# Kernel tuning notes

Hardware: AMD Instinct MI355X
Metric: run time of the kernel (lower is better)

Reference implementation:

```python
import jax, jax.numpy as jnp
import numpy as np

HEAD_DIM = 128
N_HEADS = 16
N_KV_HEADS = 4
ROPE_BASE = 10000.0
TRAIN_SEQ_LEN = 1024


def _rotary_cos_sin(seq_len, rd, base=ROPE_BASE, train_len=TRAIN_SEQ_LEN):
    # NTK-style base scaling when seq_len exceeds training length (matches Rotary.forward)
    if seq_len > train_len:
        scale = seq_len / train_len
        base = base * scale ** (rd / (rd - 2))
    inv_freq = 1.0 / base ** (np.arange(0, rd, 2, dtype=np.float32) / rd)
    freqs = np.outer(np.arange(seq_len, dtype=np.float32), inv_freq)  # [T, rd/2]
    cos = jnp.asarray(np.cos(freqs))[None, :, None, :]  # [1,T,1,rd/2]
    sin = jnp.asarray(np.sin(freqs))[None, :, None, :]
    return cos, sin


def _apply_rotary(x, cos, sin):
    h = x.shape[-1] // 2
    x1, x2 = x[..., :h], x[..., h:]
    return jnp.concatenate((x1 * cos + x2 * sin, -x1 * sin + x2 * cos), axis=-1)


def _rms_norm(x):
    eps = jnp.finfo(x.dtype).eps
    return x * jax.lax.rsqrt(jnp.mean(x * x, axis=-1, keepdims=True) + eps)


def setup_inputs() -> dict:
    key = jax.random.key(0)
    ks = jax.random.split(key, 6)
    B, T, D = 4, 2048, 2048
    x = jax.random.normal(ks[0], (B, T, D), dtype=jnp.float32)
    q_w = jax.random.normal(ks[1], (D, D), dtype=jnp.float32) * 0.02
    k_w = jax.random.normal(ks[2], (N_KV_HEADS * HEAD_DIM, D), dtype=jnp.float32) * 0.02
    v_w = jax.random.normal(ks[3], (N_KV_HEADS * HEAD_DIM, D), dtype=jnp.float32) * 0.02
    out_w = jax.random.normal(ks[4], (D, D), dtype=jnp.float32) * 0.02
    q_gain = jnp.ones((N_HEADS,), dtype=jnp.float32)
    return {"x": x, "q_w": q_w, "k_w": k_w, "v_w": v_w, "out_w": out_w, "q_gain": q_gain}


def reference(x, q_w, k_w, v_w, out_w, q_gain):
    B, T, D = x.shape
    q = (x @ q_w.T).reshape(B, T, N_HEADS, HEAD_DIM)
    k = (x @ k_w.T).reshape(B, T, N_KV_HEADS, HEAD_DIM)
    v = (x @ v_w.T).reshape(B, T, N_KV_HEADS, HEAD_DIM)
    q = _rms_norm(q)
    k = _rms_norm(k)
    cos, sin = _rotary_cos_sin(T, HEAD_DIM)
    q = _apply_rotary(q, cos, sin)
    k = _apply_rotary(k, cos, sin)
    q = q * q_gain[None, None, :, None]
    # GQA: expand kv heads (repeat_interleave semantics)
    rep = N_HEADS // N_KV_HEADS
    k = jnp.repeat(k, rep, axis=2)  # [B,T,H,D]
    v = jnp.repeat(v, rep, axis=2)
    scale = 1.0 / jnp.sqrt(jnp.asarray(HEAD_DIM, dtype=x.dtype))
    scores = jnp.einsum("bthd,bshd->bhts", q, k) * scale  # [B,H,T,T]
    causal = jnp.tril(jnp.ones((T, T), dtype=bool))
    scores = jnp.where(causal[None, None], scores, jnp.asarray(-jnp.inf, dtype=scores.dtype))
    w = jax.nn.softmax(scores, axis=-1)
    y = jnp.einsum("bhts,bshd->bthd", w, v).reshape(B, T, D)
    return y @ out_w.T
```

## Files before the change

### kernel.cpp

```cpp
#include <hip/hip_runtime.h>
#include <hip/hip_bf16.h>
#include <math.h>

#define HEAD_DIM 128
#define NH 16
#define NKV 4
#define BB 4
#define TT 2048
#define DD 2048
#define ROWS (BB*TT)

typedef unsigned short u16;
typedef unsigned int u32;
typedef __attribute__((ext_vector_type(8))) short short8;
typedef __attribute__((ext_vector_type(4))) float f32x4;
typedef __attribute__((ext_vector_type(16))) float f32x16;
typedef __attribute__((ext_vector_type(4))) unsigned short u16x4;

__device__ __forceinline__ float bf2f(u16 u) {
    union { unsigned int i; float f; } v; v.i = ((unsigned int)u) << 16; return v.f;
}
__device__ __forceinline__ u16 f2bf(float f) {
    union { float f; unsigned int i; } v; v.f = f;
    unsigned int r = v.i + 0x7FFFu + ((v.i >> 16) & 1u);
    return (u16)(r >> 16);
}
__device__ __forceinline__ f32x4 mfma16(short8 a, short8 b, f32x4 c) {
    return __builtin_amdgcn_mfma_f32_16x16x32_bf16(a, b, c, 0, 0, 0);
}
__device__ __forceinline__ f32x16 mfma32(short8 a, short8 b, f32x16 c) {
    return __builtin_amdgcn_mfma_f32_32x32x16_bf16(a, b, c, 0, 0, 0);
}
__device__ __forceinline__ f32x16 zero16() {
    f32x16 z;
    #pragma unroll
    for (int i = 0; i < 16; ++i) z[i] = 0.f;
    return z;
}
__device__ __forceinline__ void gload_lds16(const u16* g, u16* l) {
    __builtin_amdgcn_global_load_lds(
        (const __attribute__((address_space(1))) unsigned int*)(const void*)g,
        (__attribute__((address_space(3))) unsigned int*)(void*)l, 16, 0, 0);
}

__global__ __launch_bounds__(256)
void cast_f2b(const float* __restrict__ in, u16* __restrict__ out, int n)
{
    int i = (blockIdx.x * 256 + threadIdx.x) * 4;
    if (i >= n) return;
    float4 v = *(const float4*)(in + i);
    u16x4 o;
    o.x = f2bf(v.x); o.y = f2bf(v.y); o.z = f2bf(v.z); o.w = f2bf(v.w);
    *(u16x4*)(out + i) = o;
}

__global__ __launch_bounds__(256)
void prep_all(const float* __restrict__ x,  const float* __restrict__ qw,
              const float* __restrict__ kw, const float* __restrict__ vw,
              u16* __restrict__ xh, u16* __restrict__ wq, u16* __restrict__ wkv,
              float* __restrict__ cs, float* __restrict__ sn, float base)
{
    const int bid = blockIdx.x, tid = threadIdx.x;
    if (bid < 22528) {
        const float* src; u16* dst; int i4;
        if (bid < 16384)      { src = x;  dst = xh;            i4 = bid; }
        else if (bid < 20480) { src = qw; dst = wq;            i4 = bid - 16384; }
        else if (bid < 21504) { src = kw; dst = wkv;           i4 = bid - 20480; }
        else                  { src = vw; dst = wkv + 1048576; i4 = bid - 21504; }
        int i = (i4 * 256 + tid) * 4;
        float4 v = *(const float4*)(src + i);
        u16x4 o;
        o.x = f2bf(v.x); o.y = f2bf(v.y); o.z = f2bf(v.z); o.w = f2bf(v.w);
        *(u16x4*)(dst + i) = o;
    } else {
        int idx = (bid - 22528) * 256 + tid;
        int t = idx >> 6;
        int d = idx & 63;
        float inv = powf(base, -(float)(2 * d) / 128.0f);
        float f = (float)t * inv;
        cs[idx] = cosf(f);
        sn[idx] = sinf(f);
    }
}

__global__ __launch_bounds__(256)
void transpose_v(const u16* __restrict__ vbh, u16* __restrict__ vtb)
{
    __shared__ u16 tile[64][72];
    const int tb = blockIdx.x;
    const int db = blockIdx.y;
    const int z  = blockIdx.z;
    const int tid = threadIdx.x;

    {
        const int r = tid >> 2, cq = tid & 3;
        const u16* src = vbh + ((size_t)(((z >> 2) * TT + tb * 64 + r) * NKV + (z & 3))) * 128
                             + db * 64 + cq * 16;
        short8 s0 = *(const short8*)(src);
        short8 s1 = *(const short8*)(src + 8);
        #pragma unroll
        for (int e = 0; e < 8; ++e) tile[r][cq * 16 + e]     = (u16)s0[e];
        #pragma unroll
        for (int e = 0; e < 8; ++e) tile[r][cq * 16 + 8 + e] = (u16)s1[e];
    }
    __syncthreads();
    {
        const int d = tid >> 2, tq = tid & 3;
        __attribute__((aligned(16))) u16 tmp[16];
        #pragma unroll
        for (int e = 0; e < 16; ++e) {
            int esw = (e & 3) | ((e & 4) << 1) | ((e & 8) >> 1);
            tmp[e] = tile[tq * 16 + esw][d];
        }
        u16* dst = vtb + (((size_t)(z * (TT / 64) + tb) * 128 + (db * 64 + d)) << 6) + tq * 16;
        *(short8*)(dst)     = ((short8*)tmp)[0];
        *(short8*)(dst + 8) = ((short8*)tmp)[1];
    }
}

template<int BN, int OUTMODE>
__global__ __launch_bounds__(512, 2)
void gemm256(const u16* __restrict__ A, const u16* __restrict__ W,
             void* __restrict__ C0, void* __restrict__ C1,
             const float* __restrict__ CS, const float* __restrict__ SN,
             const float* __restrict__ GAIN, float PRE)
{
    constexpr int WN    = (BN == 256) ? 4 : 2;
    constexpr int MR    = (BN == 256) ? 8 : 4;
    constexpr int WROW  = (BN == 256) ? 128 : 64;
    constexpr int NT    = DD / 64;
    constexpr int NBI   = (BN == 256) ? 4 : 2;
    constexpr int BPR   = BN / 16;

    __shared__ u16 LDSall[2 * 128 * 128 + 2 * (BN / 2) * 128];
    __shared__ float Sred[1024];
    u16* AsL = LDSall;
    u16* BsL = LDSall + 2 * 128 * 128;

    const int tid = threadIdx.x;
    const int w = tid >> 6, l = tid & 63;
    const int lq = l & 15, lg = l >> 4;
    const int wmi = (WN == 4) ? (w >> 2) : (w >> 1);
    const int wni = w & (WN - 1);

    int bmi, bni;
    {
        const int bid = blockIdx.x;
        const int wg = (bid & 7) * 32 + (bid >> 3);
        const int st = wg >> 2, wi = wg & 3;
        const int sty = st >> 2, stx = st & 3;
        bmi = sty * 2 + (wi >> 1);
        bni = stx * 2 + (wi & 1);
    }
    const int bm = bmi * 256, bn = bni * BN;

    const int sro = l >> 4;
    const int sch = l & 15;

    f32x4 acc[MR][4];
    #pragma unroll
    for (int m = 0; m < MR; ++m)
        #pragma unroll
        for (int n = 0; n < 4; ++n) acc[m][n] = (f32x4){0.f, 0.f, 0.f, 0.f};

    auto stage = [&](int buf, int t) {
        const size_t ko = (size_t)t * 64;
        u16* Ad = AsL + buf * (128 * 128);
        u16* Bd = BsL + buf * ((BN / 2) * 128);
        #pragma unroll
        for (int j = 0; j < 4; ++j) {
            int rp = w * 16 + j * 4 + sro;
            int cg = sch ^ (rp & 15);
            gload_lds16(A + (size_t)(bm + 2 * rp + (cg >> 3)) * DD + ko + (cg & 7) * 8,
                        Ad + (w * 16 + j * 4) * 128);
        }
        #pragma unroll
        for (int j = 0; j < NBI; ++j) {
            int rp = w * BPR + j * 4 + sro;
            int cg = sch ^ (rp & 15);
            gload_lds16(W + (size_t)(bn + 2 * rp + (cg >> 3)) * DD + ko + (cg & 7) * 8,
                        Bd + (w * BPR + j * 4) * 128);
        }
    };

    stage(0, 0);
    stage(1, 1);
    if constexpr (BN == 256) asm volatile("s_waitcnt vmcnt(8)" ::: "memory");
    else                     asm volatile("s_waitcnt vmcnt(6)" ::: "memory");
    __builtin_amdgcn_s_barrier();
    __builtin_amdgcn_sched_barrier(0);

    const int mh = lq >> 1;
    const int e8 = (lq & 1) << 3;
    for (int t = 0; t < NT; ++t) {
        const int buf = t & 1;
        const u16* Ab = AsL + buf * (128 * 128);
        const u16* Bb = BsL + buf * ((BN / 2) * 128);
        #pragma unroll
        for (int ks = 0; ks < 2; ++ks) {
            short8 af[MR], bf[4];
            #pragma unroll
            for (int m = 0; m < MR; ++m) {
                int rp = wmi * (WROW / 2) + m * 8 + mh;
                af[m] = *(const short8*)(Ab + rp * 128 + (((e8 + ks * 4 + lg) ^ (rp & 15)) << 3));
            }
            #pragma unroll
            for (int n = 0; n < 4; ++n) {
                int rp = wni * 32 + n * 8 + mh;
                bf[n] = *(const short8*)(Bb + rp * 128 + (((e8 + ks * 4 + lg) ^ (rp & 15)) << 3));
            }
            __builtin_amdgcn_s_setprio(1);
            #pragma unroll
            for (int m = 0; m < MR; ++m)
                #pragma unroll
                for (int n = 0; n < 4; ++n)
                    acc[m][n] = mfma16(af[m], bf[n], acc[m][n]);
            __builtin_amdgcn_s_setprio(0);
        }

        if (t + 1 < NT) {
            __builtin_amdgcn_sched_barrier(0);
            __builtin_amdgcn_s_barrier();
            if (t + 2 < NT) {
                stage(buf, t + 2);
                if constexpr (BN == 256) asm volatile("s_waitcnt vmcnt(8)" ::: "memory");
                else                     asm volatile("s_waitcnt vmcnt(6)" ::: "memory");
            } else {
                asm volatile("s_waitcnt vmcnt(0)" ::: "memory");
            }
            __builtin_amdgcn_s_barrier();
            __builtin_amdgcn_sched_barrier(0);
        }
    }

    if constexpr (OUTMODE == 2) {
        #pragma unroll
        for (int m = 0; m < MR; ++m) {
            int grow = bm + wmi * WROW + m * 16 + lg * 4;
            #pragma unroll
            for (int n = 0; n < 4; ++n) {
                int col = wni * 64 + n * 16 + lq;
                #pragma unroll
                for (int q = 0; q < 4; ++q)
                    ((float*)C0)[(size_t)(grow + q) * 2048 + bn + col] = acc[m][n][q];
            }
        }
    } else {
        const bool isK = (OUTMODE == 3) ? true : (bni < 4);
        u16* E = LDSall;
        constexpr int RS = (OUTMODE == 3) ? 256 : 128;
        constexpr int CM = (OUTMODE == 3) ? 31 : 15;

        if (isK) {
            __syncthreads();
            #pragma unroll
            for (int m = 0; m < MR; ++m) {
                f32x4 ps = acc[m][0] * acc[m][0];
                #pragma unroll
                for (int n = 1; n < 4; ++n) ps += acc[m][n] * acc[m][n];
                #pragma unroll
                for (int q = 0; q < 4; ++q) {
                    float v = ps[q];
                    v += __shfl_xor(v, 1, 64);
                    v += __shfl_xor(v, 2, 64);
                    v += __shfl_xor(v, 4, 64);
                    v += __shfl_xor(v, 8, 64);
                    if (lq == 0) {
                        int lr = m * 16 + lg * 4 + q;
                        if constexpr (OUTMODE == 3)
                            Sred[wmi * 512 + lr * 4 + (wni >> 1) * 2 + (wni & 1)] = v;
                        else
                            Sred[wmi * 128 + lr * 2 + (wni & 1)] = v;
                    }
                }
            }
            __syncthreads();
            #pragma unroll
            for (int m = 0; m < MR; ++m) {
                f32x4 rs4;
                #pragma unroll
                for (int q = 0; q < 4; ++q) {
                    int lr = m * 16 + lg * 4 + q;
                    float tot;
                    if constexpr (OUTMODE == 3)
                        tot = Sred[wmi * 512 + lr * 4 + (wni >> 1) * 2]
                            + Sred[wmi * 512 + lr * 4 + (wni >> 1) * 2 + 1];
                    else
                        tot = Sred[wmi * 128 + lr * 2]
                            + Sred[wmi * 128 + lr * 2 + 1];
                    rs4[q] = 1.0f / sqrtf(tot * (1.0f / 128.0f) + 1.1920929e-7f);
                }
                #pragma unroll
                for (int n = 0; n < 4; ++n) {
                    #pragma unroll
                    for (int q = 0; q < 4; ++q) {
                        int rloc = wmi * WROW + m * 16 + lg * 4 + q;
                        int col  = wni * 64 + n * 16 + lq;
                        int eoff = rloc * RS + ((((col >> 3) ^ (rloc & CM)) << 3) | (col & 7));
                        E[eoff] = f2bf(acc[m][n][q] * rs4[q]);
                    }
                }
            }
            __syncthreads();
            constexpr int NU = (OUTMODE == 3) ? 8 : 4;
            #pragma unroll
            for (int u = 0; u < NU; ++u) {
                int gu = u * 512 + tid;
                int pair = gu & 7;
                int rloc = (gu >> 3) & 255;
                int hsub = (OUTMODE == 3) ? (gu >> 11) : 0;
                int d0 = pair * 8;
                int cl = hsub * 128 + d0;
                int ch = cl + 64;
                short8 lo = *(const short8*)&E[rloc * RS + (((cl >> 3) ^ (rloc & CM)) << 3)];
                short8 hi2 = *(const short8*)&E[rloc * RS + (((ch >> 3) ^ (rloc & CM)) << 3)];
                int grow = bm + rloc;
                int t = grow & 2047, bb = grow >> 11;
                float4 c0 = *(const float4*)&CS[t * 64 + d0];
                float4 c1 = *(const float4*)&CS[t * 64 + d0 + 4];
                float4 s0 = *(const float4*)&SN[t * 64 + d0];
                float4 s1 = *(const float4*)&SN[t * 64 + d0 + 4];
                float cc[8] = {c0.x, c0.y, c0.z, c0.w, c1.x, c1.y, c1.z, c1.w};
                float ssv[8] = {s0.x, s0.y, s0.z, s0.w, s1.x, s1.y, s1.z, s1.w};
                float g = 1.f;
                size_t obase;
                if constexpr (OUTMODE == 3) {
                    int h = (bn >> 7) + hsub;
                    g = GAIN[h] * PRE;
                    obase = ((size_t)(bb * NH + h) * TT + t) << 7;
                } else {
                    obase = ((size_t)(bb * NKV + bni) * TT + t) << 7;
                }
                union { u16 e[8]; short8 s8; } o1, o2;
                #pragma unroll
                for (int e = 0; e < 8; ++e) {
                    float x1 = bf2f((u16)lo[e]);
                    float x2 = bf2f((u16)hi2[e]);
                    o1.e[e] = f2bf((x1 * cc[e] + x2 * ssv[e]) * g);
                    o2.e[e] = f2bf((-x1 * ssv[e] + x2 * cc[e]) * g);
                }
                *(short8*)((u16*)C0 + obase + d0)      = o1.s8;
                *(short8*)((u16*)C0 + obase + 64 + d0) = o2.s8;
            }
        } else {
            #pragma unroll
            for (int m = 0; m < MR; ++m) {
                int growb = bm + wmi * WROW + m * 16 + lg * 4;
                #pragma unroll
                for (int n = 0; n < 4; ++n) {
                    int cg = bn + wni * 64 + n * 16 + lq - 512;
                    #pragma unroll
                    for (int q = 0; q < 4; ++q)
                        ((u16*)C1)[(size_t)(growb + q) * 512 + cg] = f2bf(acc[m][n][q]);
                }
            }
        }
    }
}

__global__ __launch_bounds__(256, 2)
void attn_mfma(const u16* __restrict__ qg,
               const u16* __restrict__ kg,
               const u16* __restrict__ vtg,
               u16* __restrict__ yg)
{
    __shared__ u16 Ks[2][64 * 128];
    __shared__ u16 Vs[2][64 * 128];

    const int tid = threadIdx.x, wid = tid >> 6, l = tid & 63;
    const int lq = l & 31, hi = l >> 5, hi4 = hi << 2;

    const int bid = blockIdx.x;
    const int xcd  = bid & 7;
    const int s    = bid >> 3;
    const int gsub = s >> 5;
    const int hh   = (s >> 3) & 3;
    const int fold = s & 7;
    const int g    = xcd + (gsub << 3);
    const int b = g >> 2, kvh = g & 3;
    const int h = kvh * 4 + hh;

    const u16* kg_bh = kg + (((size_t)g * TT) << 7);
    const u16* vt_bh = vtg + (size_t)g * (TT / 64) * 8192;
    const u16* q_bh  = qg + (((size_t)(b * NH + h) * TT) << 7);

    const int nta = 2 * fold + 2;
    const int NT  = 34;

    const int sro = l >> 4;
    const int sch = l & 15;

    auto stage = [&](int buf, int kt) {
        #pragma unroll
        for (int i = 0; i < 4; ++i) {
            int kr = wid * 16 + i * 4 + sro;
            int cgk = sch ^ (kr & 15);
            gload_lds16(kg_bh + (((size_t)(kt * 64 + kr)) << 7) + (cgk << 3),
                        &Ks[buf][(wid * 16 + i * 4) << 7]);
            int rp = wid * 16 + i * 4 + sro;
            int cgv = sch ^ (rp & 15);
            gload_lds16(vt_bh + (size_t)kt * 8192 + ((2 * rp + (cgv >> 3)) << 6) + ((cgv & 7) << 3),
                        &Vs[buf][(wid * 16 + i * 4) << 7]);
        }
    };

    stage(0, 0);
    stage(1, 1);
    asm volatile("s_waitcnt vmcnt(8)" ::: "memory");
    __builtin_amdgcn_s_barrier();
    __builtin_amdgcn_sched_barrier(0);

    int step = 0;

    for (int seg = 0; seg < 2; ++seg) {
        const int qblk = seg ? (15 - fold) : fold;
        const int nseg = seg ? (32 - 2 * fold) : nta;
        const int qrow = qblk * 128 + wid * 32 + lq;
        const int diag = (qblk * 128 + wid * 32) >> 6;

        const u16* qptr = q_bh + ((size_t)qrow << 7) + hi * 8;
        short8 qf[8];
        #pragma unroll
        for (int q = 0; q < 8; ++q)
            qf[q] = *(const short8*)(qptr + q * 16);

        f32x16 accO[4];
        #pragma unroll
        for (int d = 0; d < 4; ++d) accO[d] = zero16();
        float m2 = -1e30f, lr = 0.f;

        for (int kt = 0; kt < nseg; ++kt, ++step) {
            const int buf = step & 1;

            if (kt <= diag) {
                const u16* Kc = Ks[buf];
                f32x16 accS0 = zero16(), accS1 = zero16();
                __builtin_amdgcn_s_setprio(1);
                #pragma unroll
                for (int ss = 0; ss < 8; ++ss) {
                    int c = ((2 * ss + hi) ^ (lq & 15)) << 3;
                    short8 kf0 = *(const short8*)(Kc + (lq << 7) + c);
                    accS0 = mfma32(kf0, qf[ss], accS0);
                    short8 kf1 = *(const short8*)(Kc + ((32 + lq) << 7) + c);
                    accS1 = mfma32(kf1, qf[ss], accS1);
                }
                __builtin_amdgcn_s_setprio(0);

                float p[32];
                if (kt == diag) {
                    #pragma unroll
                    for (int r = 0; r < 16; ++r) {
                        int key0 = kt * 64 + (r & 3) + 8 * (r >> 2) + hi4;
                        p[r]      = (key0      > qrow) ? -INFINITY : accS0[r];
                        p[16 + r] = (key0 + 32 > qrow) ? -INFINITY : accS1[r];
                    }
                } else {
                    #pragma unroll
                    for (int r = 0; r < 16; ++r) { p[r] = accS0[r]; p[16 + r] = accS1[r]; }
                }

                float t16[16];
                #pragma unroll
                for (int i = 0; i < 16; ++i) t16[i] = fmaxf(p[i], p[i + 16]);
                #pragma unroll
                for (int i = 0; i < 8; ++i) t16[i] = fmaxf(t16[i], t16[i + 8]);
                #pragma unroll
                for (int i = 0; i < 4; ++i) t16[i] = fmaxf(t16[i], t16[i + 4]);
                float pm = fmaxf(fmaxf(t16[0], t16[1]), fmaxf(t16[2], t16[3]));
                pm = fmaxf(pm, __shfl_xor(pm, 32, 64));

                float mn = m2;
                if (!__all(pm - m2 <= 8.0f)) {
                    mn = fmaxf(m2, pm);
                    float al = exp2f(m2 - mn);
                    lr *= al;
                    #pragma unroll
                    for (int d = 0; d < 4; ++d) accO[d] *= al;
                    m2 = mn;
                }

                #pragma unroll
                for (int r = 0; r < 32; ++r) p[r] = exp2f(p[r] - mn);
                #pragma unroll
                for (int i = 0; i < 16; ++i) t16[i] = p[i] + p[i + 16];
                #pragma unroll
                for (int i = 0; i < 8; ++i) t16[i] += t16[i + 8];
                #pragma unroll
                for (int i = 0; i < 4; ++i) t16[i] += t16[i + 4];
                float rs = (t16[0] + t16[1]) + (t16[2] + t16[3]);
                rs += __shfl_xor(rs, 32, 64);
                lr += rs;

                short8 pfrag[4];
                #pragma unroll
                for (int kb = 0; kb < 2; ++kb)
                    #pragma unroll
                    for (int c = 0; c < 2; ++c) {
                        union { u32 u[4]; short8 s8; } f;
                        #pragma unroll
                        for (int j = 0; j < 4; ++j) {
                            __hip_bfloat162 hb = __float22bfloat162_rn(
                                make_float2(p[kb * 16 + 8 * c + 2 * j],
                                            p[kb * 16 + 8 * c + 2 * j + 1]));
                            f.u[j] = *reinterpret_cast<u32*>(&hb);
                        }
                        pfrag[kb * 2 + c] = f.s8;
                    }

                const u16* Vc = Vs[buf];
                const int rv = lq >> 1;
                const int ev = (lq & 1) << 3;
                #pragma unroll
                for (int d = 0; d < 4; ++d) {
                    const u16* vr8 = Vc + ((d * 16 + rv) << 7);
                    short8 vf0 = *(const short8*)(vr8 + (((ev + 0 + hi) ^ rv) << 3));
                    short8 vf1 = *(const short8*)(vr8 + (((ev + 2 + hi) ^ rv) << 3));
                    short8 vf2 = *(const short8*)(vr8 + (((ev + 4 + hi) ^ rv) << 3));
                    short8 vf3 = *(const short8*)(vr8 + (((ev + 6 + hi) ^ rv) << 3));
                    __builtin_amdgcn_s_setprio(1);
                    accO[d] = mfma32(vf0, pfrag[0], accO[d]);
                    accO[d] = mfma32(vf1, pfrag[1], accO[d]);
                    accO[d] = mfma32(vf2, pfrag[2], accO[d]);
                    accO[d] = mfma32(vf3, pfrag[3], accO[d]);
                    __builtin_amdgcn_s_setprio(0);
                }
            }

            if (step + 1 < NT) {
                __builtin_amdgcn_sched_barrier(0);
                __builtin_amdgcn_s_barrier();
                if (step + 2 < NT) {
                    int tn = step + 2;
                    stage(buf, (tn < nta) ? tn : tn - nta);
                    asm volatile("s_waitcnt vmcnt(8)" ::: "memory");
                } else {
                    asm volatile("s_waitcnt vmcnt(0)" ::: "memory");
                }
                __builtin_amdgcn_s_barrier();
                __builtin_amdgcn_sched_barrier(0);
            }
        }

        float inv = 1.0f / lr;
        u16* yrow = yg + ((size_t)((b * TT + qrow) * NH + h) << 7);
        #pragma unroll
        for (int d = 0; d < 4; ++d)
            #pragma unroll
            for (int r = 0; r < 4; ++r) {
                u16x4 o;
                #pragma unroll
                for (int q = 0; q < 4; ++q) o[q] = f2bf(accO[d][4 * r + q] * inv);
                *(u16x4*)(yrow + d * 32 + 8 * r + hi4) = o;
            }
    }
}

extern "C" void kernel_launch(void* const* d_in, const int* in_sizes, int n_in,
                              void* d_out, int out_size, void* d_ws, size_t ws_size,
                              hipStream_t stream)
{
    const float* x      = (const float*)d_in[0];
    const float* q_w    = (const float*)d_in[1];
    const float* k_w    = (const float*)d_in[2];
    const float* v_w    = (const float*)d_in[3];
    const float* out_w  = (const float*)d_in[4];
    const float* q_gain = (const float*)d_in[5];
    float* out = (float*)d_out;

    char* ws = (char*)d_ws;
    u16* q2   = (u16*)(ws);
    u16* xh   = (u16*)(ws + 33554432ull);
    u16* wqkv = (u16*)(ws + 67108864ull);
    u16* vtb  = (u16*)(ws + 79691776ull);
    u16* vbh  = (u16*)(ws + 88080384ull);
    float* cs = (float*)(ws + 96468992ull);
    float* sn = cs + TT * 64;
    u16* wq   = wqkv;
    u16* wkv  = wqkv + 4194304;
    u16* kk   = wqkv;
    u16* wout = vbh;
    u16* y    = xh;

    dim3 blk(256);

    double base = 10000.0 * pow((double)TT / 1024.0, 128.0 / 126.0);
    prep_all<<<dim3(23040), blk, 0, stream>>>(x, q_w, k_w, v_w, xh, wq, wkv,
                                              cs, sn, (float)base);

    const float pre_q = 0.08838834764831845f * 1.4426950408889634f;
    gemm256<256, 3><<<dim3(256), dim3(512), 0, stream>>>(xh, wq, q2, nullptr,
                                                         cs, sn, q_gain, pre_q);
    gemm256<128, 4><<<dim3(256), dim3(512), 0, stream>>>(xh, wkv, kk, vbh,
                                                         cs, sn, nullptr, 0.f);

    transpose_v<<<dim3(TT / 64, 2, BB * NKV), blk, 0, stream>>>(vbh, vtb);

    cast_f2b<<<dim3(4096), blk, 0, stream>>>(out_w, wout, DD * DD);

    attn_mfma<<<dim3(512), blk, 0, stream>>>(q2, kk, vtb, y);

    gemm256<256, 2><<<dim3(256), dim3(512), 0, stream>>>(y, wout, out, nullptr,
                                                         nullptr, nullptr, nullptr, 0.f);
}
```

Measured before the change: 320.9 us.

## Replace 256-wide GEMM tiles with 128x128 tiles and 256-thread blocks

Swaps the 512-thread GEMM that used 256x256 (or 256x128) output tiles with a 256-thread kernel using 128x128 tiles, a K-step of 32, and a new swizzled LDS layout. Grid sizes grow accordingly (1024/512 blocks), and the launch bound allows four blocks per CU. The aim is more blocks in flight and better occupancy and latency hiding. The cost is lower per-block data reuse, more global and L2 traffic, and twice as many barrier steps along K. The RMSNorm/rotary epilogue is simplified to one head per block.

```diff
diff --git a/kernel.cpp b/kernel.cpp
--- a/kernel.cpp
+++ b/kernel.cpp
@@ -118,113 +118,102 @@
     }
 }
 
-template<int BN, int OUTMODE>
-__global__ __launch_bounds__(512, 2)
-void gemm256(const u16* __restrict__ A, const u16* __restrict__ W,
+template<int OUTMODE, int NBX>
+__global__ __launch_bounds__(256, 4)
+void gemm128(const u16* __restrict__ A, const u16* __restrict__ W,
              void* __restrict__ C0, void* __restrict__ C1,
              const float* __restrict__ CS, const float* __restrict__ SN,
              const float* __restrict__ GAIN, float PRE)
 {
-    constexpr int WN    = (BN == 256) ? 4 : 2;
-    constexpr int MR    = (BN == 256) ? 8 : 4;
-    constexpr int WROW  = (BN == 256) ? 128 : 64;
-    constexpr int NT    = DD / 64;
-    constexpr int NBI   = (BN == 256) ? 4 : 2;
-    constexpr int BPR   = BN / 16;
-
-    __shared__ u16 LDSall[2 * 128 * 128 + 2 * (BN / 2) * 128];
-    __shared__ float Sred[1024];
+    constexpr int NT = DD / 32;
+    __shared__ u16 LDSall[16384];
+    __shared__ float Sred[256];
     u16* AsL = LDSall;
-    u16* BsL = LDSall + 2 * 128 * 128;
+    u16* BsL = LDSall + 8192;
 
     const int tid = threadIdx.x;
     const int w = tid >> 6, l = tid & 63;
     const int lq = l & 15, lg = l >> 4;
-    const int wmi = (WN == 4) ? (w >> 2) : (w >> 1);
-    const int wni = w & (WN - 1);
+    const int wmi = w >> 1, wni = w & 1;
 
     int bmi, bni;
     {
         const int bid = blockIdx.x;
-        const int wg = (bid & 7) * 32 + (bid >> 3);
-        const int st = wg >> 2, wi = wg & 3;
-        const int sty = st >> 2, stx = st & 3;
-        bmi = sty * 2 + (wi >> 1);
-        bni = stx * 2 + (wi & 1);
-    }
-    const int bm = bmi * 256, bn = bni * BN;
-
-    const int sro = l >> 4;
-    const int sch = l & 15;
-
-    f32x4 acc[MR][4];
+        constexpr int nblk = NBX * 64;
+        constexpr int per = nblk >> 3;
+        const int wg = (bid & 7) * per + (bid >> 3);
+        const int st = wg >> 4, wi = wg & 15;
+        constexpr int stw = NBX >> 2;
+        const int sty = st / stw, stx = st - sty * stw;
+        bmi = sty * 4 + (wi >> 2);
+        bni = stx * 4 + (wi & 3);
+    }
+    const int bm = bmi << 7, bn = bni << 7;
+
+    const int rpl = l >> 3;
+    const int sc  = l & 7;
+
+    f32x4 acc[4][4];
     #pragma unroll
-    for (int m = 0; m < MR; ++m)
+    for (int m = 0; m < 4; ++m)
         #pragma unroll
         for (int n = 0; n < 4; ++n) acc[m][n] = (f32x4){0.f, 0.f, 0.f, 0.f};
 
     auto stage = [&](int buf, int t) {
-        const size_t ko = (size_t)t * 64;
-        u16* Ad = AsL + buf * (128 * 128);
-        u16* Bd = BsL + buf * ((BN / 2) * 128);
-        #pragma unroll
-        for (int j = 0; j < 4; ++j) {
-            int rp = w * 16 + j * 4 + sro;
-            int cg = sch ^ (rp & 15);
-            gload_lds16(A + (size_t)(bm + 2 * rp + (cg >> 3)) * DD + ko + (cg & 7) * 8,
-                        Ad + (w * 16 + j * 4) * 128);
-        }
-        #pragma unroll
-        for (int j = 0; j < NBI; ++j) {
-            int rp = w * BPR + j * 4 + sro;
-            int cg = sch ^ (rp & 15);
-            gload_lds16(W + (size_t)(bn + 2 * rp + (cg >> 3)) * DD + ko + (cg & 7) * 8,
-                        Bd + (w * BPR + j * 4) * 128);
+        const size_t ko = (size_t)t * 32;
+        u16* Ad = AsL + buf * 4096;
+        u16* Bd = BsL + buf * 4096;
+        #pragma unroll
+        for (int j = 0; j < 2; ++j) {
+            int rp = w * 16 + j * 8 + rpl;
+            int cg = sc ^ (rp & 7);
+            gload_lds16(A + (size_t)(bm + 2 * rp + (cg >> 2)) * DD + ko + (cg & 3) * 8,
+                        Ad + (w * 16 + j * 8) * 64);
+            int cg2 = sc ^ (rp & 7);
+            gload_lds16(W + (size_t)(bn + 2 * rp + (cg2 >> 2)) * DD + ko + (cg2 & 3) * 8,
+                        Bd + (w * 16 + j * 8) * 64);
         }
     };
 
     stage(0, 0);
     stage(1, 1);
-    if constexpr (BN == 256) asm volatile("s_waitcnt vmcnt(8)" ::: "memory");
-    else                     asm volatile("s_waitcnt vmcnt(6)" ::: "memory");
+    asm volatile("s_waitcnt vmcnt(4)" ::: "memory");
     __builtin_amdgcn_s_barrier();
     __builtin_amdgcn_sched_barrier(0);
 
-    const int mh = lq >> 1;
-    const int e8 = (lq & 1) << 3;
     for (int t = 0; t < NT; ++t) {
         const int buf = t & 1;
-        const u16* Ab = AsL + buf * (128 * 128);
-        const u16* Bb = BsL + buf * ((BN / 2) * 128);
-        #pragma unroll
-        for (int ks = 0; ks < 2; ++ks) {
-            short8 af[MR], bf[4];
-            #pragma unroll
-            for (int m = 0; m < MR; ++m) {
-                int rp = wmi * (WROW / 2) + m * 8 + mh;
-                af[m] = *(const short8*)(Ab + rp * 128 + (((e8 + ks * 4 + lg) ^ (rp & 15)) << 3));
-            }
-            #pragma unroll
-            for (int n = 0; n < 4; ++n) {
-                int rp = wni * 32 + n * 8 + mh;
-                bf[n] = *(const short8*)(Bb + rp * 128 + (((e8 + ks * 4 + lg) ^ (rp & 15)) << 3));
-            }
-            __builtin_amdgcn_s_setprio(1);
-            #pragma unroll
-            for (int m = 0; m < MR; ++m)
-                #pragma unroll
-                for (int n = 0; n < 4; ++n)
-                    acc[m][n] = mfma16(af[m], bf[n], acc[m][n]);
-            __builtin_amdgcn_s_setprio(0);
-        }
+        const u16* Ab = AsL + buf * 4096;
+        const u16* Bb = BsL + buf * 4096;
+        short8 af[4], bf[4];
+        #pragma unroll
+        for (int m = 0; m < 4; ++m) {
+            int row = wmi * 64 + m * 16 + lq;
+            int rp = row >> 1;
+            int ch = (((row & 1) << 2) + lg) ^ (rp & 7);
+            af[m] = *(const short8*)(Ab + rp * 64 + ch * 8);
+        }
+        #pragma unroll
+        for (int n = 0; n < 4; ++n) {
+            int row = wni * 64 + n * 16 + lq;
+            int rp = row >> 1;
+            int ch = (((row & 1) << 2) + lg) ^ (rp & 7);
+            bf[n] = *(const short8*)(Bb + rp * 64 + ch * 8);
+        }
+        __builtin_amdgcn_s_setprio(1);
+        #pragma unroll
+        for (int m = 0; m < 4; ++m)
+            #pragma unroll
+            for (int n = 0; n < 4; ++n)
+                acc[m][n] = mfma16(af[m], bf[n], acc[m][n]);
+        __builtin_amdgcn_s_setprio(0);
 
         if (t + 1 < NT) {
             __builtin_amdgcn_sched_barrier(0);
             __builtin_amdgcn_s_barrier();
             if (t + 2 < NT) {
                 stage(buf, t + 2);
-                if constexpr (BN == 256) asm volatile("s_waitcnt vmcnt(8)" ::: "memory");
-                else                     asm volatile("s_waitcnt vmcnt(6)" ::: "memory");
+                asm volatile("s_waitcnt vmcnt(4)" ::: "memory");
             } else {
                 asm volatile("s_waitcnt vmcnt(0)" ::: "memory");
             }
@@ -235,26 +224,24 @@
 
     if constexpr (OUTMODE == 2) {
         #pragma unroll
-        for (int m = 0; m < MR; ++m) {
-            int grow = bm + wmi * WROW + m * 16 + lg * 4;
+        for (int m = 0; m < 4; ++m) {
+            int grow = bm + wmi * 64 + m * 16 + lg * 4;
             #pragma unroll
             for (int n = 0; n < 4; ++n) {
-                int col = wni * 64 + n * 16 + lq;
+                int col = bn + wni * 64 + n * 16 + lq;
                 #pragma unroll
                 for (int q = 0; q < 4; ++q)
-                    ((float*)C0)[(size_t)(grow + q) * 2048 + bn + col] = acc[m][n][q];
+                    ((float*)C0)[(size_t)(grow + q) * 2048 + col] = acc[m][n][q];
             }
         }
     } else {
         const bool isK = (OUTMODE == 3) ? true : (bni < 4);
         u16* E = LDSall;
-        constexpr int RS = (OUTMODE == 3) ? 256 : 128;
-        constexpr int CM = (OUTMODE == 3) ? 31 : 15;
 
         if (isK) {
             __syncthreads();
             #pragma unroll
-            for (int m = 0; m < MR; ++m) {
+            for (int m = 0; m < 4; ++m) {
                 f32x4 ps = acc[m][0] * acc[m][0];
                 #pragma unroll
                 for (int n = 1; n < 4; ++n) ps += acc[m][n] * acc[m][n];
@@ -266,54 +253,41 @@
                     v += __shfl_xor(v, 4, 64);
                     v += __shfl_xor(v, 8, 64);
                     if (lq == 0) {
-                        int lr = m * 16 + lg * 4 + q;
-                        if constexpr (OUTMODE == 3)
-                            Sred[wmi * 512 + lr * 4 + (wni >> 1) * 2 + (wni & 1)] = v;
-                        else
-                            Sred[wmi * 128 + lr * 2 + (wni & 1)] = v;
+                        int lr = wmi * 64 + m * 16 + lg * 4 + q;
+                        Sred[lr * 2 + wni] = v;
                     }
                 }
             }
             __syncthreads();
             #pragma unroll
-            for (int m = 0; m < MR; ++m) {
+            for (int m = 0; m < 4; ++m) {
                 f32x4 rs4;
                 #pragma unroll
                 for (int q = 0; q < 4; ++q) {
-                    int lr = m * 16 + lg * 4 + q;
-                    float tot;
-                    if constexpr (OUTMODE == 3)
-                        tot = Sred[wmi * 512 + lr * 4 + (wni >> 1) * 2]
-                            + Sred[wmi * 512 + lr * 4 + (wni >> 1) * 2 + 1];
-                    else
-                        tot = Sred[wmi * 128 + lr * 2]
-                            + Sred[wmi * 128 + lr * 2 + 1];
+                    int lr = wmi * 64 + m * 16 + lg * 4 + q;
+                    float tot = Sred[lr * 2] + Sred[lr * 2 + 1];
                     rs4[q] = 1.0f / sqrtf(tot * (1.0f / 128.0f) + 1.1920929e-7f);
                 }
                 #pragma unroll
                 for (int n = 0; n < 4; ++n) {
                     #pragma unroll
                     for (int q = 0; q < 4; ++q) {
-                        int rloc = wmi * WROW + m * 16 + lg * 4 + q;
+                        int rloc = wmi * 64 + m * 16 + lg * 4 + q;
                         int col  = wni * 64 + n * 16 + lq;
-                        int eoff = rloc * RS + ((((col >> 3) ^ (rloc & CM)) << 3) | (col & 7));
+                        int eoff = rloc * 128 + ((((col >> 3) ^ (rloc & 15)) << 3) | (col & 7));
                         E[eoff] = f2bf(acc[m][n][q] * rs4[q]);
                     }
                 }
             }
             __syncthreads();
-            constexpr int NU = (OUTMODE == 3) ? 8 : 4;
-            #pragma unroll
-            for (int u = 0; u < NU; ++u) {
-                int gu = u * 512 + tid;
+            #pragma unroll
+            for (int u = 0; u < 4; ++u) {
+                int gu = u * 256 + tid;
                 int pair = gu & 7;
-                int rloc = (gu >> 3) & 255;
-                int hsub = (OUTMODE == 3) ? (gu >> 11) : 0;
+                int rloc = gu >> 3;
                 int d0 = pair * 8;
-                int cl = hsub * 128 + d0;
-                int ch = cl + 64;
-                short8 lo = *(const short8*)&E[rloc * RS + (((cl >> 3) ^ (rloc & CM)) << 3)];
-                short8 hi2 = *(const short8*)&E[rloc * RS + (((ch >> 3) ^ (rloc & CM)) << 3)];
+                short8 lo  = *(const short8*)&E[rloc * 128 + (((d0 >> 3) ^ (rloc & 15)) << 3)];
+                short8 hi2 = *(const short8*)&E[rloc * 128 + ((((d0 + 64) >> 3) ^ (rloc & 15)) << 3)];
                 int grow = bm + rloc;
                 int t = grow & 2047, bb = grow >> 11;
                 float4 c0 = *(const float4*)&CS[t * 64 + d0];
@@ -325,7 +299,7 @@
                 float g = 1.f;
                 size_t obase;
                 if constexpr (OUTMODE == 3) {
-                    int h = (bn >> 7) + hsub;
+                    int h = bn >> 7;
                     g = GAIN[h] * PRE;
                     obase = ((size_t)(bb * NH + h) * TT + t) << 7;
                 } else {
@@ -344,8 +318,8 @@
             }
         } else {
             #pragma unroll
-            for (int m = 0; m < MR; ++m) {
-                int growb = bm + wmi * WROW + m * 16 + lg * 4;
+            for (int m = 0; m < 4; ++m) {
+                int growb = bm + wmi * 64 + m * 16 + lg * 4;
                 #pragma unroll
                 for (int n = 0; n < 4; ++n) {
                     int cg = bn + wni * 64 + n * 16 + lq - 512;
@@ -588,10 +562,10 @@
                                               cs, sn, (float)base);
 
     const float pre_q = 0.08838834764831845f * 1.4426950408889634f;
-    gemm256<256, 3><<<dim3(256), dim3(512), 0, stream>>>(xh, wq, q2, nullptr,
-                                                         cs, sn, q_gain, pre_q);
-    gemm256<128, 4><<<dim3(256), dim3(512), 0, stream>>>(xh, wkv, kk, vbh,
-                                                         cs, sn, nullptr, 0.f);
+    gemm128<3, 16><<<dim3(1024), blk, 0, stream>>>(xh, wq, q2, nullptr,
+                                                   cs, sn, q_gain, pre_q);
+    gemm128<4, 8><<<dim3(512), blk, 0, stream>>>(xh, wkv, kk, vbh,
+                                                 cs, sn, nullptr, 0.f);
 
     transpose_v<<<dim3(TT / 64, 2, BB * NKV), blk, 0, stream>>>(vbh, vtb);
 
@@ -599,6 +573,6 @@
 
     attn_mfma<<<dim3(512), blk, 0, stream>>>(q2, kk, vtb, y);
 
-    gemm256<256, 2><<<dim3(256), dim3(512), 0, stream>>>(y, wout, out, nullptr,
-                                                         nullptr, nullptr, nullptr, 0.f);
-}
+    gemm128<2, 16><<<dim3(1024), blk, 0, stream>>>(y, wout, out, nullptr,
+                                                   nullptr, nullptr, nullptr, 0.f);
+}
```

Result: slower. 338.3 us (+5.4%).

## Add ping-pong pipelined output-projection GEMM with split B loads and priority

Applied to the files above, without the earlier changes.

Replaces the generic templated GEMM for the output projection with a specialised kernel. It uses a three-slot LDS ring, interleaves the A and B global-to-LDS staging between two MFMA halves, raises wave priority around the MFMA bursts, and uses an XCD-aware tile mapping. The goal is to hide global load latency behind compute and cut barrier stalls. The cost is duplicated code, and the hand-tuned waitcnt and barrier placement could hurt if the schedule is mistimed.

```diff
diff --git a/kernel.cpp b/kernel.cpp
--- a/kernel.cpp
+++ b/kernel.cpp
@@ -358,6 +358,134 @@
     }
 }
 
+__global__ __launch_bounds__(512, 1)
+void gemm256p(const u16* __restrict__ A, const u16* __restrict__ W,
+              float* __restrict__ C0)
+{
+    constexpr int NT = DD / 32;
+    __shared__ u16 As[3][128 * 64];
+    __shared__ u16 Bs[3][128 * 64];
+
+    const int tid = threadIdx.x;
+    const int w = tid >> 6, l = tid & 63;
+    const int lq = l & 15, lg = l >> 4;
+    const int wmi = w >> 2, wni = w & 3;
+
+    int bmi, bni;
+    {
+        const int bid = blockIdx.x;
+        const int wg = (bid & 7) * 32 + (bid >> 3);
+        const int st = wg >> 2, wi = wg & 3;
+        const int sty = st >> 2, stx = st & 3;
+        bmi = sty * 2 + (wi >> 1);
+        bni = stx * 2 + (wi & 1);
+    }
+    const int bm = bmi * 256, bn = bni * 256;
+
+    const int rpl = l >> 3;
+    const int sc  = l & 7;
+
+    f32x4 acc[8][4];
+    #pragma unroll
+    for (int m = 0; m < 8; ++m)
+        #pragma unroll
+        for (int n = 0; n < 4; ++n) acc[m][n] = (f32x4){0.f, 0.f, 0.f, 0.f};
+
+    auto stageA = [&](int slot, int t) {
+        const size_t ko = (size_t)t * 32;
+        u16* Ad = As[slot];
+        #pragma unroll
+        for (int j = 0; j < 2; ++j) {
+            int rp = w * 16 + j * 8 + rpl;
+            int cg = sc ^ (rp & 7);
+            gload_lds16(A + (size_t)(bm + 2 * rp + (cg >> 2)) * DD + ko + (cg & 3) * 8,
+                        Ad + (w * 16 + j * 8) * 64);
+        }
+    };
+    auto stageB = [&](int slot, int t) {
+        const size_t ko = (size_t)t * 32;
+        u16* Bd = Bs[slot];
+        #pragma unroll
+        for (int j = 0; j < 2; ++j) {
+            int rp = w * 16 + j * 8 + rpl;
+            int cg = sc ^ (rp & 7);
+            gload_lds16(W + (size_t)(bn + 2 * rp + (cg >> 2)) * DD + ko + (cg & 3) * 8,
+                        Bd + (w * 16 + j * 8) * 64);
+        }
+    };
+
+    stageA(0, 0); stageB(0, 0);
+    stageA(1, 1); stageB(1, 1);
+    asm volatile("s_waitcnt vmcnt(4)" ::: "memory");
+    __builtin_amdgcn_s_barrier();
+
+    int slot = 0;
+    for (int t = 0; t < NT; ++t) {
+        const u16* Ab = As[slot];
+        const u16* Bb = Bs[slot];
+        const int wslot = (slot + 2 >= 3) ? slot - 1 : slot + 2;
+
+        short8 af[8], bf0[2];
+        #pragma unroll
+        for (int m = 0; m < 8; ++m) {
+            int row = wmi * 128 + m * 16 + lq;
+            int rp = row >> 1;
+            int ch = (((row & 1) << 2) + lg) ^ (rp & 7);
+            af[m] = *(const short8*)(Ab + rp * 64 + ch * 8);
+        }
+        #pragma unroll
+        for (int n = 0; n < 2; ++n) {
+            int row = wni * 64 + n * 16 + lq;
+            int rp = row >> 1;
+            int ch = (((row & 1) << 2) + lg) ^ (rp & 7);
+            bf0[n] = *(const short8*)(Bb + rp * 64 + ch * 8);
+        }
+        if (t + 2 < NT) stageA(wslot, t + 2);
+        __builtin_amdgcn_s_barrier();
+        __builtin_amdgcn_s_setprio(1);
+        #pragma unroll
+        for (int m = 0; m < 8; ++m) {
+            acc[m][0] = mfma16(af[m], bf0[0], acc[m][0]);
+            acc[m][1] = mfma16(af[m], bf0[1], acc[m][1]);
+        }
+        __builtin_amdgcn_s_setprio(0);
+
+        short8 bf1[2];
+        #pragma unroll
+        for (int n = 0; n < 2; ++n) {
+            int row = wni * 64 + (n + 2) * 16 + lq;
+            int rp = row >> 1;
+            int ch = (((row & 1) << 2) + lg) ^ (rp & 7);
+            bf1[n] = *(const short8*)(Bb + rp * 64 + ch * 8);
+        }
+        if (t + 2 < NT) stageB(wslot, t + 2);
+        __builtin_amdgcn_s_setprio(1);
+        #pragma unroll
+        for (int m = 0; m < 8; ++m) {
+            acc[m][2] = mfma16(af[m], bf1[0], acc[m][2]);
+            acc[m][3] = mfma16(af[m], bf1[1], acc[m][3]);
+        }
+        __builtin_amdgcn_s_setprio(0);
+        if (t + 2 < NT) asm volatile("s_waitcnt vmcnt(4)" ::: "memory");
+        else            asm volatile("s_waitcnt vmcnt(0)" ::: "memory");
+        __builtin_amdgcn_s_barrier();
+
+        slot = (slot == 2) ? 0 : slot + 1;
+    }
+
+    #pragma unroll
+    for (int m = 0; m < 8; ++m) {
+        int grow = bm + wmi * 128 + m * 16 + lg * 4;
+        #pragma unroll
+        for (int n = 0; n < 4; ++n) {
+            int col = bn + wni * 64 + n * 16 + lq;
+            #pragma unroll
+            for (int q = 0; q < 4; ++q)
+                C0[(size_t)(grow + q) * 2048 + col] = acc[m][n][q];
+        }
+    }
+}
+
 __global__ __launch_bounds__(256, 2)
 void attn_mfma(const u16* __restrict__ qg,
                const u16* __restrict__ kg,
@@ -599,6 +727,5 @@
 
     attn_mfma<<<dim3(512), blk, 0, stream>>>(q2, kk, vtb, y);
 
-    gemm256<256, 2><<<dim3(256), dim3(512), 0, stream>>>(y, wout, out, nullptr,
-                                                         nullptr, nullptr, nullptr, 0.f);
-}
+    gemm256p<<<dim3(256), dim3(512), 0, stream>>>(y, wout, out);
+}
```

New measurement: 321.8 us. Within noise of the previous version (+0.3%).
